# Kernel optimization log

Hardware: AMD Instinct MI355X
Metric: run time of the kernel (lower is better)

## Reference

```python
import jax, jax.numpy as jnp
import numpy as np

B, T, V, E, H, C = 128, 256, 50000, 300, 512, 11
START, STOP = 9, 10
NEG = -100000.0


def _lstm_dir(x, mask, w_ih, w_hh, b_ih, b_hh, reverse):
    # x: [B,T,D]; precompute input-to-gate projection for all timesteps
    gx = jnp.einsum('btd,gd->btg', x, w_ih) + b_ih + b_hh
    m = mask
    if reverse:
        gx = gx[:, ::-1]
        m = m[:, ::-1]
    Bc = x.shape[0]
    Hh = w_hh.shape[1]

    def step(carry, inp):
        h, c = carry
        g, mt = inp
        gates = g + h @ w_hh.T  # [B,4H]
        i, f, gg, o = jnp.split(gates, 4, axis=-1)
        i = jax.nn.sigmoid(i)
        f = jax.nn.sigmoid(f)
        o = jax.nn.sigmoid(o)
        gg = jnp.tanh(gg)
        c_new = f * c + i * gg
        h_new = o * jnp.tanh(c_new)
        mt = mt[:, None]
        h = jnp.where(mt, h_new, h)  # packed-sequence semantics: hold state on pads
        c = jnp.where(mt, c_new, c)
        return (h, c), h

    init = (jnp.zeros((Bc, Hh), x.dtype), jnp.zeros((Bc, Hh), x.dtype))
    _, hs = jax.lax.scan(step, init, (gx.transpose(1, 0, 2), m.T))
    hs = hs.transpose(1, 0, 2)
    if reverse:
        hs = hs[:, ::-1]
    # pad_packed_sequence zeroes padded positions
    return hs * mask[..., None].astype(x.dtype)


def _encode(tokens, mask, embeddings, params):
    x = embeddings[tokens]
    for (wif, whf, bif, bhf, wir, whr, bir, bhr) in params:
        fwd = _lstm_dir(x, mask, wif, whf, bif, bhf, False)
        bwd = _lstm_dir(x, mask, wir, whr, bir, bhr, True)
        x = jnp.concatenate([fwd, bwd], -1)
    return x


def _viterbi(emis, mask, transitions, seq_len):
    def vstep(scores, inp):
        emi, mt = inp
        cand = scores[:, :, None] + transitions[None]  # [B,C,C]
        bt = jnp.argmax(cand, axis=1)
        new = jnp.max(cand, axis=1) + emi
        return jnp.where(mt[:, None], new, scores), bt

    scores0 = jnp.zeros_like(emis[:, 0, :])
    final, backtrack = jax.lax.scan(vstep, scores0, (emis.transpose(1, 0, 2), mask.T))
    final = final + transitions[:, STOP][None]
    best_last = jnp.argmax(final, axis=-1)  # [B]

    ls = jnp.arange(emis.shape[1] - 1, -1, -1)

    def btstep(cur, inp):
        bt_l, l = inp
        emit = jnp.where(l < seq_len, cur, 0)  # pad tail with 0 as in original
        prev = jnp.take_along_axis(bt_l, cur[:, None], axis=1)[:, 0]
        cur = jnp.where((l >= 1) & (l <= seq_len - 1), prev, cur)
        return cur, emit

    _, emits = jax.lax.scan(btstep, best_last, (backtrack[::-1], ls))
    return emits[::-1].T  # [B,T]


def _nll(emis, tags, mask, transitions, seq_len):
    # CRF forward algorithm (replicates original init with -1e5 full scores)
    def fstep(scores, inp):
        emi, mt = inp
        new = jax.nn.logsumexp(scores[:, :, None] + emi[:, None, :] + transitions[None], axis=1)
        return jnp.where(mt[:, None], new, scores), None

    scores0 = jnp.full_like(emis[:, 0, :], NEG)
    final, _ = jax.lax.scan(fstep, scores0, (emis.transpose(1, 0, 2), mask.T))
    fwd_score = jax.nn.logsumexp(final + transitions[:, STOP][None], axis=-1, keepdims=True)

    em_sc = jnp.take_along_axis(emis, tags[..., None], -1)[..., 0]  # [B,T]
    y_aug = jnp.concatenate([jnp.full((tags.shape[0], 1), START, tags.dtype), tags], 1)
    tr_sc = transitions[y_aug[:, :-1], y_aug[:, 1:]]  # [B,T]
    last_tag = jnp.take_along_axis(y_aug, seq_len[:, None], 1)
    last_tr = transitions[last_tag[:, 0], STOP][:, None]
    mf = mask.astype(emis.dtype)
    gold = (mf * (em_sc + tr_sc)).sum(-1, keepdims=True) + last_tr
    return (fwd_score - gold).mean()


def setup_inputs() -> dict:
    key = jax.random.key(0)
    ks = iter(jax.random.split(key, 40))
    sl = jax.random.randint(next(ks), (B,), 1, T + 1)
    sl = -jnp.sort(-sl.at[0].set(T))  # descending, max == T (pack_padded requirement)
    mask = jnp.arange(T)[None, :] < sl[:, None]
    tokens = jax.random.randint(next(ks), (B, T), 0, V)
    tags = jax.random.randint(next(ks), (B, T), 0, 9)
    s = 1.0 / float(np.sqrt(H))

    def u(shape):
        return jax.random.uniform(next(ks), shape, jnp.float32, -s, s)

    inp = dict(tokens=tokens, seq_len=sl, mask=mask, tags=tags,
               embeddings=jax.random.normal(next(ks), (V, E), jnp.float32) * 0.1)
    G = 4 * H
    for li, d in enumerate([E, 2 * H]):
        for suf in ['', 'r']:
            inp[f'w_ih_l{li}{suf}'] = u((G, d))
            inp[f'w_hh_l{li}{suf}'] = u((G, H))
            inp[f'b_ih_l{li}{suf}'] = u((G,))
            inp[f'b_hh_l{li}{suf}'] = u((G,))
    inp['fc_w'] = u((C, 2 * H))
    inp['fc_b'] = u((C,))
    tr = jax.random.normal(next(ks), (C, C), jnp.float32)
    inp['transitions'] = tr.at[START, :].set(-1.0).at[:, STOP].set(-1.0)
    return inp


def reference(tokens, seq_len, mask, tags, embeddings,
              w_ih_l0, w_hh_l0, b_ih_l0, b_hh_l0,
              w_ih_l0r, w_hh_l0r, b_ih_l0r, b_hh_l0r,
              w_ih_l1, w_hh_l1, b_ih_l1, b_hh_l1,
              w_ih_l1r, w_hh_l1r, b_ih_l1r, b_hh_l1r,
              fc_w, fc_b, transitions):
    params = [(w_ih_l0, w_hh_l0, b_ih_l0, b_hh_l0, w_ih_l0r, w_hh_l0r, b_ih_l0r, b_hh_l0r),
              (w_ih_l1, w_hh_l1, b_ih_l1, b_hh_l1, w_ih_l1r, w_hh_l1r, b_ih_l1r, b_hh_l1r)]
    out = _encode(tokens, mask, embeddings, params)  # [B,T,2H]
    emis = jnp.einsum('bth,ch->btc', out, fc_w) + fc_b  # CRF fc (dropout=eval no-op)
    pred = _viterbi(emis, mask, transitions, seq_len)
    loss = _nll(emis, tags, mask, transitions, seq_len)
    return pred, loss
```

## Files before the change

### kernel.cpp

```cpp
#include <hip/hip_runtime.h>
#include <hip/hip_bf16.h>
#include <hip/hip_fp16.h>

#define BB   128
#define TT   256
#define EE   300
#define KP0  320
#define HH   512
#define GG   2048
#define NC   11
#define MM   (BB*TT)
#define START_TAG 9
#define STOP_TAG  10
#define NEGV (-100000.0f)

typedef _Float16 h2_t __attribute__((ext_vector_type(2)));
typedef _Float16 h4_t __attribute__((ext_vector_type(4)));
typedef _Float16 h8_t __attribute__((ext_vector_type(8)));
typedef float    f4_t __attribute__((ext_vector_type(4)));

__device__ __forceinline__ float sigf(float x) {
    return __builtin_amdgcn_rcpf(1.0f + __expf(-x));
}
__device__ __forceinline__ float tanh_fast(float x) {
    float e = __expf(2.0f * x);
    return 1.0f - 2.0f * __builtin_amdgcn_rcpf(e + 1.0f);
}

__device__ __forceinline__ void gload_lds16(const void* g, void* l) {
    __builtin_amdgcn_global_load_lds(
        (const __attribute__((address_space(1))) void*)(unsigned long long)(uintptr_t)g,
        (__attribute__((address_space(3))) void*)(unsigned int)(uintptr_t)l,
        16, 0, 0);
}

__global__ __launch_bounds__(256) void init_kernel(float* out, int* flags) {
    int t = threadIdx.x;
    if (t == 0) out[MM] = 0.0f;
    for (int i = t; i < 1024; i += 256) flags[i] = 0;
}

__global__ __launch_bounds__(256) void conv_pad_kernel(const float* __restrict__ W,
                                                       _Float16* __restrict__ O,
                                                       int K, int Kp4, int total4) {
    int idx = blockIdx.x * 256 + threadIdx.x;
    if (idx >= total4) return;
    int r = idx / Kp4, c4 = idx % Kp4, c = c4 * 4;
    h4_t v;
    if (c < K) {
        float4 f = *(const float4*)(W + (size_t)r * K + c);
        v[0] = (_Float16)f.x; v[1] = (_Float16)f.y; v[2] = (_Float16)f.z; v[3] = (_Float16)f.w;
    } else {
        v[0] = v[1] = v[2] = v[3] = (_Float16)0.0f;
    }
    *(h4_t*)(O + (size_t)r * (Kp4 * 4) + c) = v;
}

__global__ __launch_bounds__(256) void embed16_kernel(const int* __restrict__ tok,
                                                      const float* __restrict__ emb,
                                                      _Float16* __restrict__ x0,
                                                      int total4) {
    int idx = blockIdx.x * 256 + threadIdx.x;
    if (idx >= total4) return;
    int m = idx / (KP0 / 4), c4 = idx % (KP0 / 4), c = c4 * 4;
    h4_t v;
    if (c < EE) {
        float4 f = *(const float4*)(emb + (size_t)tok[m] * EE + c);
        v[0] = (_Float16)f.x; v[1] = (_Float16)f.y; v[2] = (_Float16)f.z; v[3] = (_Float16)f.w;
    } else {
        v[0] = v[1] = v[2] = v[3] = (_Float16)0.0f;
    }
    *(h4_t*)(x0 + (size_t)m * KP0 + c) = v;
}

__global__ __launch_bounds__(256) void gemm_bt_kernel(const _Float16* __restrict__ A,
                                                      const _Float16* __restrict__ Wf,
                                                      const float* __restrict__ b1,
                                                      const float* __restrict__ b2,
                                                      _Float16* __restrict__ C,
                                                      int Kp) {
    __shared__ __align__(16) char smem[36864];
    _Float16* As = (_Float16*)smem;
    _Float16* Bs = (_Float16*)(smem + 16384);
    const int tid = threadIdx.x;
    const int m0 = blockIdx.y * 128, n0 = blockIdx.x * 128;
    const int wv = tid >> 6, lane = tid & 63;
    const int wm = wv & 1, wn = wv >> 1;
    const int col = lane & 15, quad = lane >> 4;
    const int rb = lane >> 3;
    const int cb = (lane & 7) * 8;

    f4_t acc[4][4];
#pragma unroll
    for (int i = 0; i < 4; ++i)
#pragma unroll
        for (int j = 0; j < 4; ++j) acc[i][j] = (f4_t){0.f, 0.f, 0.f, 0.f};

    for (int k0 = 0; k0 < Kp; k0 += 64) {
#pragma unroll
        for (int c = 0; c < 4; ++c) {
            int slab = c * 32 + wv * 8;
            gload_lds16(A  + (size_t)(m0 + slab + rb) * Kp + k0 + cb, As + slab * 64);
            gload_lds16(Wf + (size_t)(n0 + slab + rb) * Kp + k0 + cb, Bs + slab * 64);
        }
        __syncthreads();
#pragma unroll
        for (int kk = 0; kk < 2; ++kk) {
            h8_t af[4], bf[4];
#pragma unroll
            for (int i = 0; i < 4; ++i) {
                af[i] = *(const h8_t*)(As + (wm * 64 + i * 16 + col) * 64 + kk * 32 + quad * 8);
                bf[i] = *(const h8_t*)(Bs + (wn * 64 + i * 16 + col) * 64 + kk * 32 + quad * 8);
            }
#pragma unroll
            for (int mi = 0; mi < 4; ++mi)
#pragma unroll
                for (int ni = 0; ni < 4; ++ni)
                    acc[mi][ni] = __builtin_amdgcn_mfma_f32_16x16x32_f16(af[mi], bf[ni], acc[mi][ni], 0, 0, 0);
        }
        __syncthreads();
    }

    _Float16* Ct = (_Float16*)smem;
#pragma unroll
    for (int ni = 0; ni < 4; ++ni) {
        int n = n0 + wn * 64 + ni * 16 + col;
        float bias = b1[n] + b2[n];
#pragma unroll
        for (int mi = 0; mi < 4; ++mi) {
#pragma unroll
            for (int r = 0; r < 4; ++r) {
                int mrow = wm * 64 + mi * 16 + quad * 4 + r;
                Ct[mrow * 136 + wn * 64 + ni * 16 + col] = (_Float16)(acc[mi][ni][r] + bias);
            }
        }
    }
    __syncthreads();
    {
        int row = tid >> 1, half = tid & 1;
#pragma unroll
        for (int cc2 = 0; cc2 < 8; ++cc2) {
            h8_t v = *(const h8_t*)(Ct + row * 136 + half * 64 + cc2 * 8);
            *(h8_t*)(C + (size_t)(m0 + row) * GG + n0 + half * 64 + cc2 * 8) = v;
        }
    }
}

__global__ __launch_bounds__(256, 1) void lstm_rec3_kernel(
        const _Float16* __restrict__ gx_f, const _Float16* __restrict__ gx_r,
        const float* __restrict__ whh_f, const float* __restrict__ whh_r,
        const int* __restrict__ seqlen, int c0, int nbg,
        _Float16* __restrict__ hs, _Float16* __restrict__ hbuf, int* __restrict__ flags) {
    extern __shared__ _Float16 Wlds[];
    _Float16* hstage = Wlds + 32768;

    const int wg = blockIdx.x;
    const int gs = wg & 15;
    const int grp = wg >> 4;
    const int bg = grp % nbg;
    const int dir = grp / nbg;
    const _Float16* gx = dir ? gx_r : gx_f;
    const float* W = dir ? whh_r : whh_f;
    int* myFlags = flags + grp * 16;
    _Float16* hb = hbuf + (size_t)grp * 2 * 16384;

    const int tid = threadIdx.x;
    const int wv = tid >> 6, lane = tid & 63;
    const int mt = wv & 1;
    const int p  = wv >> 1;
    const int col = lane & 15, quad = lane >> 4;

    for (int e = tid; e < 4096; e += 256) {
        int ln = e & 63, kc = (e >> 6) & 15, nt = e >> 10;
        int pp = nt >> 1;
        int n_in_pair = ((nt & 1) << 4) + (ln & 15);
        int gt = n_in_pair >> 3, jj = n_in_pair & 7;
        int R = gt * 512 + gs * 16 + pp * 8 + jj;
        int k = kc * 32 + (ln >> 4) * 8;
        const float4* src = (const float4*)(W + (size_t)R * 512 + k);
        float4 f0 = src[0], f1 = src[1];
        h8_t v;
        v[0] = (_Float16)f0.x; v[1] = (_Float16)f0.y; v[2] = (_Float16)f0.z; v[3] = (_Float16)f0.w;
        v[4] = (_Float16)f1.x; v[5] = (_Float16)f1.y; v[6] = (_Float16)f1.z; v[7] = (_Float16)f1.w;
        *(h8_t*)(Wlds + (size_t)e * 8) = v;
    }
    __syncthreads();

    h8_t Bf0[16], Bf1[16];
#pragma unroll
    for (int kc = 0; kc < 16; ++kc) {
        Bf0[kc] = *(const h8_t*)(Wlds + (((p * 2 + 0) * 16 + kc) * 64 + lane) * 8);
        Bf1[kc] = *(const h8_t*)(Wlds + (((p * 2 + 1) * 16 + kc) * 64 + lane) * 8);
    }

    const int maxsl = seqlen[c0 + bg * 32];
    int sl_r[4];
#pragma unroll
    for (int r = 0; r < 4; ++r) sl_r[r] = seqlen[c0 + bg * 32 + mt * 16 + quad * 4 + r];

    const int jglob = gs * 16 + p * 8 + (col & 7);
    const int hi = col >> 3;

    _Float16 pg0[4], pg1[4];
#pragma unroll
    for (int r = 0; r < 4; ++r) {
        pg0[r] = (_Float16)0.0f; pg1[r] = (_Float16)0.0f;
        if (0 < sl_r[r]) {
            int tm = dir ? (sl_r[r] - 1) : 0;
            int b_loc = bg * 32 + mt * 16 + quad * 4 + r;
            size_t base = ((size_t)(b_loc * TT + tm)) * GG;
            pg0[r] = gx[base + hi * 512 + jglob];
            pg1[r] = gx[base + 1024 + hi * 512 + jglob];
        }
    }

    if (tid < 64) {
        int m = tid >> 1, half = tid & 1;
        h8_t z = {};
        const _Float16* dst = hb + 16384 + m * 512 + gs * 16 + half * 8;
        asm volatile("global_store_dwordx4 %0, %1, off sc0 sc1" :: "v"(dst), "v"(z) : "memory");
        asm volatile("s_waitcnt vmcnt(0)" ::: "memory");
        if (tid == 0) {
            int one = 1;
            asm volatile("global_store_dword %0, %1, off sc0 sc1" :: "v"(myFlags + gs), "v"(one) : "memory");
        }
    }

    float cst[4] = {0.f, 0.f, 0.f, 0.f};
    float hst[4] = {0.f, 0.f, 0.f, 0.f};

    for (int s = 0; s < maxsl; ++s) {
        if (tid < 16) {
            const int* fp = myFlags + tid;
            int v, it = 0;
            for (;;) {
                asm volatile("global_load_dword %0, %1, off sc0 sc1\n\ts_waitcnt vmcnt(0)"
                             : "=v"(v) : "v"(fp) : "memory");
                if (v >= s + 1) break;
                if (it < 3) __builtin_amdgcn_s_sleep(1);
                else        __builtin_amdgcn_s_sleep(4);
                ++it;
            }
        }
        __syncthreads();

        const _Float16* hrd = hb + ((s + 1) & 1) * 16384;
        _Float16* hwr = hb + (s & 1) * 16384;

        h8_t a[16];
        const _Float16* ap = hrd + (mt * 16 + col) * 512 + quad * 8;
#pragma unroll
        for (int kc = 0; kc < 16; ++kc)
            asm volatile("global_load_dwordx4 %0, %1, off sc0 sc1"
                         : "=v"(a[kc]) : "v"(ap + kc * 32));
        asm volatile("s_waitcnt vmcnt(0)" ::: "memory");
        __builtin_amdgcn_sched_barrier(0);

        f4_t acc0a = {0.f, 0.f, 0.f, 0.f}, acc0b = {0.f, 0.f, 0.f, 0.f};
        f4_t acc1a = {0.f, 0.f, 0.f, 0.f}, acc1b = {0.f, 0.f, 0.f, 0.f};
#pragma unroll
        for (int kc = 0; kc < 8; ++kc) {
            acc0a = __builtin_amdgcn_mfma_f32_16x16x32_f16(a[kc], Bf0[kc], acc0a, 0, 0, 0);
            acc1a = __builtin_amdgcn_mfma_f32_16x16x32_f16(a[kc], Bf1[kc], acc1a, 0, 0, 0);
        }
#pragma unroll
        for (int kc = 8; kc < 16; ++kc) {
            acc0b = __builtin_amdgcn_mfma_f32_16x16x32_f16(a[kc], Bf0[kc], acc0b, 0, 0, 0);
            acc1b = __builtin_amdgcn_mfma_f32_16x16x32_f16(a[kc], Bf1[kc], acc1b, 0, 0, 0);
        }
        f4_t acc0 = acc0a + acc0b;
        f4_t acc1 = acc1a + acc1b;

#pragma unroll
        for (int r = 0; r < 4; ++r) {
            const bool valid = (s < sl_r[r]);
            float a0 = acc0[r] + (float)pg0[r];
            float a1 = acc1[r] + (float)pg1[r];
            float x0v = __shfl_xor(a0, 8);
            float x1v = __shfl_xor(a1, 8);
            float gi = hi ? x0v : a0;
            float gf = hi ? a0 : x0v;
            float gg2 = hi ? x1v : a1;
            float go = hi ? a1 : x1v;
            if (valid) {
                float cn = sigf(gf) * cst[r] + sigf(gi) * tanh_fast(gg2);
                cst[r] = cn;
                hst[r] = sigf(go) * tanh_fast(cn);
            }
            if (!hi)
                hstage[(mt * 16 + quad * 4 + r) * 16 + p * 8 + (col & 7)] = (_Float16)hst[r];
        }
        __syncthreads();

        if (tid < 64) {
            int m = tid >> 1, half = tid & 1;
            h8_t v = *(const h8_t*)(hstage + m * 16 + half * 8);
            const _Float16* dst = hwr + m * 512 + gs * 16 + half * 8;
            asm volatile("global_store_dwordx4 %0, %1, off sc0 sc1" :: "v"(dst), "v"(v) : "memory");
            asm volatile("s_waitcnt vmcnt(0)" ::: "memory");
            if (tid == 0) {
                int fv = s + 2;
                asm volatile("global_store_dword %0, %1, off sc0 sc1" :: "v"(myFlags + gs), "v"(fv) : "memory");
            }
        }

#pragma unroll
        for (int r = 0; r < 4; ++r) {
            const bool valid = (s < sl_r[r]);
            if (valid && !hi) {
                int b_loc = bg * 32 + mt * 16 + quad * 4 + r;
                int tm = dir ? (sl_r[r] - 1 - s) : s;
                hs[((size_t)(b_loc * TT + tm) << 10) + (dir << 9) + jglob] = (_Float16)hst[r];
            }
        }
        {
            int sn = s + 1;
#pragma unroll
            for (int r = 0; r < 4; ++r) {
                pg0[r] = (_Float16)0.0f; pg1[r] = (_Float16)0.0f;
                if (sn < sl_r[r]) {
                    int tm = dir ? (sl_r[r] - 1 - sn) : sn;
                    int b_loc = bg * 32 + mt * 16 + quad * 4 + r;
                    size_t base = ((size_t)(b_loc * TT + tm)) * GG;
                    pg0[r] = gx[base + hi * 512 + jglob];
                    pg1[r] = gx[base + 1024 + hi * 512 + jglob];
                }
            }
        }
    }
}

__global__ __launch_bounds__(256) void emis_kernel(const _Float16* __restrict__ hs,
                                                   const float* __restrict__ fc_w,
                                                   const float* __restrict__ fc_b,
                                                   float* __restrict__ emis, int n) {
    int idx = blockIdx.x * 256 + threadIdx.x;
    if (idx >= n) return;
    int m = idx / NC, cc = idx % NC;
    const h8_t* a = (const h8_t*)(hs + (size_t)m * 1024);
    const float4* w = (const float4*)(fc_w + (size_t)cc * 1024);
    float s = 0.f;
#pragma unroll 4
    for (int k = 0; k < 128; ++k) {
        h8_t x = a[k];
        float4 y0 = w[2 * k], y1 = w[2 * k + 1];
        s += (float)x[0] * y0.x + (float)x[1] * y0.y + (float)x[2] * y0.z + (float)x[3] * y0.w;
        s += (float)x[4] * y1.x + (float)x[5] * y1.y + (float)x[6] * y1.z + (float)x[7] * y1.w;
    }
    emis[idx] = s + fc_b[cc];
}

__global__ __launch_bounds__(64) void crf_kernel(const float* __restrict__ emis,
                                                 const int* __restrict__ seq_len,
                                                 const int* __restrict__ tags,
                                                 const float* __restrict__ trans,
                                                 unsigned char* __restrict__ bt,
                                                 float* __restrict__ out, int c0) {
    const int b_loc = blockIdx.x;
    const int b = c0 + b_loc;
    const int lane = threadIdx.x;
    __shared__ float tr[NC * NC];
    for (int i = lane; i < NC * NC; i += 64) tr[i] = trans[i];
    __syncthreads();
    const int sl = seq_len[b];
    const bool act = lane < NC;
    const int jj = act ? lane : 0;

    float vs = 0.0f;
    float ns = NEGV;

    for (int t = 0; t < sl; ++t) {
        float ej = act ? emis[(size_t)(b_loc * TT + t) * NC + lane] : 0.0f;
        float vmax = -1e30f, nmax = -1e30f;
        int varg = 0;
        float nsave[NC];
#pragma unroll
        for (int i = 0; i < NC; ++i) {
            float vi = __shfl(vs, i);
            float ni = __shfl(ns, i);
            float tij = tr[i * NC + jj];
            float cv = vi + tij;
            if (cv > vmax) { vmax = cv; varg = i; }
            float cn = ni + tij;
            nsave[i] = cn;
            if (cn > nmax) nmax = cn;
        }
        float ssum = 0.f;
#pragma unroll
        for (int i = 0; i < NC; ++i) ssum += expf(nsave[i] - nmax);
        if (act) {
            vs = vmax + ej;
            ns = nmax + logf(ssum) + ej;
            bt[(size_t)(b_loc * TT + t) * NC + lane] = (unsigned char)varg;
        }
    }

    float finv = act ? vs + tr[lane * NC + STOP_TAG] : -1e30f;
    float finn = act ? ns + tr[lane * NC + STOP_TAG] : -1e30f;
    float vbest = -1e30f, fmax = -1e30f;
    int barg = 0;
#pragma unroll
    for (int j = 0; j < NC; ++j) {
        float v = __shfl(finv, j);
        if (v > vbest) { vbest = v; barg = j; }
        float n = __shfl(finn, j);
        if (n > fmax) fmax = n;
    }
    float fsum = 0.f;
#pragma unroll
    for (int j = 0; j < NC; ++j) fsum += expf(__shfl(finn, j) - fmax);
    float fwd = fmax + logf(fsum);

    float gsum = 0.f;
    for (int t = lane; t < sl; t += 64) {
        int tg = tags[b * TT + t];
        int pv = (t == 0) ? START_TAG : tags[b * TT + t - 1];
        gsum += emis[(size_t)(b_loc * TT + t) * NC + tg] + tr[pv * NC + tg];
    }
#pragma unroll
    for (int off = 32; off > 0; off >>= 1) gsum += __shfl_down(gsum, off);

    if (lane == 0) {
        float gold = gsum + tr[tags[b * TT + sl - 1] * NC + STOP_TAG];
        atomicAdd(out + MM, (fwd - gold) * (1.0f / (float)BB));
        int cur = barg;
        for (int l = sl - 1; l >= 0; --l) {
            out[b * TT + l] = (float)cur;
            if (l >= 1) cur = (int)bt[(size_t)(b_loc * TT + l) * NC + cur];
        }
    }
    for (int l = sl + lane; l < TT; l += 64) out[b * TT + l] = 0.0f;
}

extern "C" void kernel_launch(void* const* d_in, const int* in_sizes, int n_in,
                              void* d_out, int out_size, void* d_ws, size_t ws_size,
                              hipStream_t stream) {
    (void)in_sizes; (void)n_in; (void)out_size;
    const int* tokens = (const int*)d_in[0];
    const int* seqlen = (const int*)d_in[1];
    const int* tags = (const int*)d_in[3];
    const float* emb = (const float*)d_in[4];
    const float* w_ih_l0  = (const float*)d_in[5];
    const float* w_hh_l0  = (const float*)d_in[6];
    const float* b_ih_l0  = (const float*)d_in[7];
    const float* b_hh_l0  = (const float*)d_in[8];
    const float* w_ih_l0r = (const float*)d_in[9];
    const float* w_hh_l0r = (const float*)d_in[10];
    const float* b_ih_l0r = (const float*)d_in[11];
    const float* b_hh_l0r = (const float*)d_in[12];
    const float* w_ih_l1  = (const float*)d_in[13];
    const float* w_hh_l1  = (const float*)d_in[14];
    const float* b_ih_l1  = (const float*)d_in[15];
    const float* b_hh_l1  = (const float*)d_in[16];
    const float* w_ih_l1r = (const float*)d_in[17];
    const float* w_hh_l1r = (const float*)d_in[18];
    const float* b_ih_l1r = (const float*)d_in[19];
    const float* b_hh_l1r = (const float*)d_in[20];
    const float* fc_w  = (const float*)d_in[21];
    const float* fc_b  = (const float*)d_in[22];
    const float* trans = (const float*)d_in[23];

    const size_t per_b = 2097152u + 524288u + 163840u + 11264u + 2816u;
    const size_t fixed = 524288u + 4096u + 2u * 1310720u + 2u * 4194304u;
    int Bc = 128;
    while (Bc > 32 && fixed + per_b * (size_t)Bc > ws_size) Bc >>= 1;

    char* ws = (char*)d_ws;
    _Float16* hbuf = (_Float16*)ws;
    int* flags = (int*)(ws + 524288u);
    _Float16* w0f = (_Float16*)(ws + 528384u);
    _Float16* w0r = (_Float16*)(ws + 528384u + 1310720u);
    _Float16* w1f = (_Float16*)(ws + 528384u + 2u * 1310720u);
    _Float16* w1r = (_Float16*)(ws + 528384u + 2u * 1310720u + 4194304u);
    char* p = ws + fixed;
    _Float16* gxf   = (_Float16*)p;   p += (size_t)Bc * 1048576u;
    _Float16* gxr   = (_Float16*)p;   p += (size_t)Bc * 1048576u;
    _Float16* hs    = (_Float16*)p;   p += (size_t)Bc * 524288u;
    _Float16* x0f16 = (_Float16*)p;   p += (size_t)Bc * 163840u;
    float* emis     = (float*)p;      p += (size_t)Bc * 11264u;
    unsigned char* bt = (unsigned char*)p;
    float* out = (float*)d_out;

    init_kernel<<<1, 256, 0, stream>>>(out, flags);
    conv_pad_kernel<<<(2048 * 80 + 255) / 256, 256, 0, stream>>>(w_ih_l0,  w0f, EE, 80, 2048 * 80);
    conv_pad_kernel<<<(2048 * 80 + 255) / 256, 256, 0, stream>>>(w_ih_l0r, w0r, EE, 80, 2048 * 80);
    conv_pad_kernel<<<(2048 * 256 + 255) / 256, 256, 0, stream>>>(w_ih_l1,  w1f, 1024, 256, 2048 * 256);
    conv_pad_kernel<<<(2048 * 256 + 255) / 256, 256, 0, stream>>>(w_ih_l1r, w1r, 1024, 256, 2048 * 256);

    const int nbg = Bc / 32;
    const int nchunk = BB / Bc;
    for (int cidx = 0; cidx < nchunk; ++cidx) {
        const int c0 = cidx * Bc;
        const int Mc = Bc * TT;
        dim3 gdim(GG / 128, Mc / 128);
        int* fl_l0 = flags + (cidx * 2 + 0) * 128;
        int* fl_l1 = flags + (cidx * 2 + 1) * 128;

        embed16_kernel<<<(Mc * 80 + 255) / 256, 256, 0, stream>>>(tokens + c0 * TT, emb, x0f16, Mc * 80);
        gemm_bt_kernel<<<gdim, 256, 0, stream>>>(x0f16, w0f, b_ih_l0,  b_hh_l0,  gxf, KP0);
        gemm_bt_kernel<<<gdim, 256, 0, stream>>>(x0f16, w0r, b_ih_l0r, b_hh_l0r, gxr, KP0);
        lstm_rec3_kernel<<<2 * nbg * 16, 256, 66560, stream>>>(
            gxf, gxr, w_hh_l0, w_hh_l0r, seqlen, c0, nbg, hs, hbuf, fl_l0);
        gemm_bt_kernel<<<gdim, 256, 0, stream>>>(hs, w1f, b_ih_l1,  b_hh_l1,  gxf, 1024);
        gemm_bt_kernel<<<gdim, 256, 0, stream>>>(hs, w1r, b_ih_l1r, b_hh_l1r, gxr, 1024);
        lstm_rec3_kernel<<<2 * nbg * 16, 256, 66560, stream>>>(
            gxf, gxr, w_hh_l1, w_hh_l1r, seqlen, c0, nbg, hs, hbuf, fl_l1);
        emis_kernel<<<(Mc * NC + 255) / 256, 256, 0, stream>>>(hs, fc_w, fc_b, emis, Mc * NC);
        crf_kernel<<<Bc, 64, 0, stream>>>(emis, seqlen, tags, trans, bt, out, c0);
    }
}
```

Before: 5.017 ms.

## Fuse prep kernels, restructure emission GEMV, keep CRF backtrack in LDS

Result: no change. 5.049 ms (+0.6%).

```diff
diff --git a/kernel.cpp b/kernel.cpp
--- a/kernel.cpp
+++ b/kernel.cpp
@@ -34,26 +34,31 @@
         16, 0, 0);
 }
 
-__global__ __launch_bounds__(256) void init_kernel(float* out, int* flags) {
-    int t = threadIdx.x;
-    if (t == 0) out[MM] = 0.0f;
-    for (int i = t; i < 1024; i += 256) flags[i] = 0;
-}
-
-__global__ __launch_bounds__(256) void conv_pad_kernel(const float* __restrict__ W,
-                                                       _Float16* __restrict__ O,
-                                                       int K, int Kp4, int total4) {
-    int idx = blockIdx.x * 256 + threadIdx.x;
-    if (idx >= total4) return;
+__global__ __launch_bounds__(256) void prep_kernel(float* out, int* flags,
+                                                   const float* __restrict__ wi0,  _Float16* __restrict__ o0,
+                                                   const float* __restrict__ wi0r, _Float16* __restrict__ o0r,
+                                                   const float* __restrict__ wi1,  _Float16* __restrict__ o1,
+                                                   const float* __restrict__ wi1r, _Float16* __restrict__ o1r) {
+    const int b = blockIdx.x, tid = threadIdx.x;
+    if (b == 0) {
+        if (tid == 0) out[MM] = 0.0f;
+        for (int i = tid; i < 1024; i += 256) flags[i] = 0;
+    }
+    const float* src; _Float16* dst; int K, Kp4, base;
+    if (b < 640)       { src = wi0;  dst = o0;  K = EE;   Kp4 = 80;  base = 0; }
+    else if (b < 1280) { src = wi0r; dst = o0r; K = EE;   Kp4 = 80;  base = 640; }
+    else if (b < 3328) { src = wi1;  dst = o1;  K = 1024; Kp4 = 256; base = 1280; }
+    else               { src = wi1r; dst = o1r; K = 1024; Kp4 = 256; base = 3328; }
+    int idx = (b - base) * 256 + tid;
     int r = idx / Kp4, c4 = idx % Kp4, c = c4 * 4;
     h4_t v;
     if (c < K) {
-        float4 f = *(const float4*)(W + (size_t)r * K + c);
+        float4 f = *(const float4*)(src + (size_t)r * K + c);
         v[0] = (_Float16)f.x; v[1] = (_Float16)f.y; v[2] = (_Float16)f.z; v[3] = (_Float16)f.w;
     } else {
         v[0] = v[1] = v[2] = v[3] = (_Float16)0.0f;
     }
-    *(h4_t*)(O + (size_t)r * (Kp4 * 4) + c) = v;
+    *(h4_t*)(dst + (size_t)r * (Kp4 * 4) + c) = v;
 }
 
 __global__ __launch_bounds__(256) void embed16_kernel(const int* __restrict__ tok,
@@ -237,8 +242,7 @@
                 asm volatile("global_load_dword %0, %1, off sc0 sc1\n\ts_waitcnt vmcnt(0)"
                              : "=v"(v) : "v"(fp) : "memory");
                 if (v >= s + 1) break;
-                if (it < 3) __builtin_amdgcn_s_sleep(1);
-                else        __builtin_amdgcn_s_sleep(4);
+                if (it >= 8) __builtin_amdgcn_s_sleep(2);
                 ++it;
             }
         }
@@ -333,33 +337,60 @@
 __global__ __launch_bounds__(256) void emis_kernel(const _Float16* __restrict__ hs,
                                                    const float* __restrict__ fc_w,
                                                    const float* __restrict__ fc_b,
-                                                   float* __restrict__ emis, int n) {
-    int idx = blockIdx.x * 256 + threadIdx.x;
-    if (idx >= n) return;
-    int m = idx / NC, cc = idx % NC;
-    const h8_t* a = (const h8_t*)(hs + (size_t)m * 1024);
-    const float4* w = (const float4*)(fc_w + (size_t)cc * 1024);
-    float s = 0.f;
-#pragma unroll 4
-    for (int k = 0; k < 128; ++k) {
-        h8_t x = a[k];
-        float4 y0 = w[2 * k], y1 = w[2 * k + 1];
-        s += (float)x[0] * y0.x + (float)x[1] * y0.y + (float)x[2] * y0.z + (float)x[3] * y0.w;
-        s += (float)x[4] * y1.x + (float)x[5] * y1.y + (float)x[6] * y1.z + (float)x[7] * y1.w;
-    }
-    emis[idx] = s + fc_b[cc];
+                                                   float* __restrict__ emis, int Mc) {
+    __shared__ __align__(16) float Wl[NC * 1024];
+    __shared__ float fb[NC];
+    const int tid = threadIdx.x;
+    {
+        const float4* s4 = (const float4*)fc_w;
+        float4* d4 = (float4*)Wl;
+        for (int i = tid; i < NC * 256; i += 256) d4[i] = s4[i];
+        if (tid < NC) fb[tid] = fc_b[tid];
+    }
+    __syncthreads();
+    const int wv = tid >> 6, lane = tid & 63;
+
+    for (int i = 0; i < 4; ++i) {
+        int m = blockIdx.x * 16 + wv * 4 + i;
+        if (m >= Mc) return;
+        const h8_t* xp = (const h8_t*)(hs + (size_t)m * 1024);
+        h8_t xa = xp[lane * 2], xb = xp[lane * 2 + 1];
+        float xf[16];
+#pragma unroll
+        for (int j = 0; j < 8; ++j) { xf[j] = (float)xa[j]; xf[8 + j] = (float)xb[j]; }
+
+        float s[NC];
+#pragma unroll
+        for (int c = 0; c < NC; ++c) {
+            const float4* wr = (const float4*)(Wl + c * 1024 + lane * 16);
+            float4 w0 = wr[0], w1 = wr[1], w2 = wr[2], w3 = wr[3];
+            s[c] = xf[0] * w0.x + xf[1] * w0.y + xf[2] * w0.z + xf[3] * w0.w
+                 + xf[4] * w1.x + xf[5] * w1.y + xf[6] * w1.z + xf[7] * w1.w
+                 + xf[8] * w2.x + xf[9] * w2.y + xf[10] * w2.z + xf[11] * w2.w
+                 + xf[12] * w3.x + xf[13] * w3.y + xf[14] * w3.z + xf[15] * w3.w;
+        }
+#pragma unroll
+        for (int off = 32; off > 0; off >>= 1)
+#pragma unroll
+            for (int c = 0; c < NC; ++c) s[c] += __shfl_down(s[c], off);
+        if (lane == 0) {
+            float* eo = emis + (size_t)m * NC;
+#pragma unroll
+            for (int c = 0; c < NC; ++c) eo[c] = s[c] + fb[c];
+        }
+    }
 }
 
 __global__ __launch_bounds__(64) void crf_kernel(const float* __restrict__ emis,
                                                  const int* __restrict__ seq_len,
                                                  const int* __restrict__ tags,
                                                  const float* __restrict__ trans,
-                                                 unsigned char* __restrict__ bt,
                                                  float* __restrict__ out, int c0) {
     const int b_loc = blockIdx.x;
     const int b = c0 + b_loc;
     const int lane = threadIdx.x;
     __shared__ float tr[NC * NC];
+    __shared__ unsigned char btl[TT * NC];
     for (int i = lane; i < NC * NC; i += 64) tr[i] = trans[i];
     __syncthreads();
     const int sl = seq_len[b];
@@ -369,8 +400,9 @@
     float vs = 0.0f;
     float ns = NEGV;
 
+    float ej_cur = act ? emis[(size_t)(b_loc * TT) * NC + lane] : 0.0f;
     for (int t = 0; t < sl; ++t) {
-        float ej = act ? emis[(size_t)(b_loc * TT + t) * NC + lane] : 0.0f;
+        float ej_next = (act && t + 1 < sl) ? emis[(size_t)(b_loc * TT + t + 1) * NC + lane] : 0.0f;
         float vmax = -1e30f, nmax = -1e30f;
         int varg = 0;
         float nsave[NC];
@@ -389,10 +421,11 @@
 #pragma unroll
         for (int i = 0; i < NC; ++i) ssum += expf(nsave[i] - nmax);
         if (act) {
-            vs = vmax + ej;
-            ns = nmax + logf(ssum) + ej;
-            bt[(size_t)(b_loc * TT + t) * NC + lane] = (unsigned char)varg;
-        }
+            vs = vmax + ej_cur;
+            ns = nmax + logf(ssum) + ej_cur;
+            btl[t * NC + lane] = (unsigned char)varg;
+        }
+        ej_cur = ej_next;
     }
 
     float finv = act ? vs + tr[lane * NC + STOP_TAG] : -1e30f;
@@ -426,7 +459,7 @@
         int cur = barg;
         for (int l = sl - 1; l >= 0; --l) {
             out[b * TT + l] = (float)cur;
-            if (l >= 1) cur = (int)bt[(size_t)(b_loc * TT + l) * NC + cur];
+            if (l >= 1) cur = (int)btl[l * NC + cur];
         }
     }
     for (int l = sl + lane; l < TT; l += 64) out[b * TT + l] = 0.0f;
@@ -478,14 +511,11 @@
     _Float16* hs    = (_Float16*)p;   p += (size_t)Bc * 524288u;
     _Float16* x0f16 = (_Float16*)p;   p += (size_t)Bc * 163840u;
     float* emis     = (float*)p;      p += (size_t)Bc * 11264u;
-    unsigned char* bt = (unsigned char*)p;
     float* out = (float*)d_out;
 
-    init_kernel<<<1, 256, 0, stream>>>(out, flags);
-    conv_pad_kernel<<<(2048 * 80 + 255) / 256, 256, 0, stream>>>(w_ih_l0,  w0f, EE, 80, 2048 * 80);
-    conv_pad_kernel<<<(2048 * 80 + 255) / 256, 256, 0, stream>>>(w_ih_l0r, w0r, EE, 80, 2048 * 80);
-    conv_pad_kernel<<<(2048 * 256 + 255) / 256, 256, 0, stream>>>(w_ih_l1,  w1f, 1024, 256, 2048 * 256);
-    conv_pad_kernel<<<(2048 * 256 + 255) / 256, 256, 0, stream>>>(w_ih_l1r, w1r, 1024, 256, 2048 * 256);
+    prep_kernel<<<5376, 256, 0, stream>>>(out, flags,
+                                          w_ih_l0, w0f, w_ih_l0r, w0r,
+                                          w_ih_l1, w1f, w_ih_l1r, w1r);
 
     const int nbg = Bc / 32;
     const int nchunk = BB / Bc;
@@ -505,7 +535,7 @@
         gemm_bt_kernel<<<gdim, 256, 0, stream>>>(hs, w1r, b_ih_l1r, b_hh_l1r, gxr, 1024);
         lstm_rec3_kernel<<<2 * nbg * 16, 256, 66560, stream>>>(
             gxf, gxr, w_hh_l1, w_hh_l1r, seqlen, c0, nbg, hs, hbuf, fl_l1);
-        emis_kernel<<<(Mc * NC + 255) / 256, 256, 0, stream>>>(hs, fc_w, fc_b, emis, Mc * NC);
-        crf_kernel<<<Bc, 64, 0, stream>>>(emis, seqlen, tags, trans, bt, out, c0);
-    }
-}
+        emis_kernel<<<Mc / 16, 256, 0, stream>>>(hs, fc_w, fc_b, emis, Mc);
+        crf_kernel<<<Bc, 64, 0, stream>>>(emis, seqlen, tags, trans, out, c0);
+    }
+}
```
